# Kernel optimization log

Hardware: AMD Instinct MI355X
Metric: run time of the kernel (lower is better)

## Reference

```python
import jax, jax.numpy as jnp
import numpy as np

SEQLS = [256, 256, 256, 256]
HEADS = 8
DIM_HEAD = 64
DIM = 512
SCALE = DIM_HEAD ** -0.5
EPS = 1e-5
# static segment-id per token position: [N]
SEG = np.repeat(np.arange(len(SEQLS)), SEQLS)


def setup_inputs() -> dict:
    key = jax.random.key(0)
    k_x, k_m, k_qkv, k_out = jax.random.split(key, 4)
    B, N = 8, sum(SEQLS)
    inner = HEADS * DIM_HEAD
    x = jax.random.normal(k_x, (B, N, DIM), dtype=jnp.float32)
    m_labels = jax.random.randint(k_m, (B, len(SEQLS)), 0, 2)
    gamma = jnp.ones((DIM,), jnp.float32)
    beta = jnp.zeros((DIM,), jnp.float32)
    w_qkv = jax.random.normal(k_qkv, (DIM, 3 * inner), jnp.float32) * (DIM ** -0.5)
    w_out = jax.random.normal(k_out, (inner, DIM), jnp.float32) * (inner ** -0.5)
    b_out = jnp.zeros((DIM,), jnp.float32)
    return {"x": x, "m_labels": m_labels, "gamma": gamma, "beta": beta,
            "w_qkv": w_qkv, "w_out": w_out, "b_out": b_out}


def reference(x, m_labels, gamma, beta, w_qkv, w_out, b_out):
    B, N, _ = x.shape
    # LayerNorm
    mu = jnp.mean(x, axis=-1, keepdims=True)
    var = jnp.var(x, axis=-1, keepdims=True)
    h = (x - mu) * jax.lax.rsqrt(var + EPS) * gamma + beta
    # QKV projection (no bias)
    qkv = h @ w_qkv  # [B, N, 3*inner]
    q, k, v = jnp.split(qkv, 3, axis=-1)
    to_heads = lambda t: t.reshape(B, N, HEADS, DIM_HEAD).transpose(0, 2, 1, 3)
    q, k, v = to_heads(q), to_heads(k), to_heads(v)  # [B, H, N, D]
    dots = jnp.einsum('bhid,bhjd->bhij', q, k) * SCALE  # [B, H, N, N]
    # modality-block additive mask: -inf on any row/col of a missing modality
    missing = (m_labels == 0)[:, SEG]  # [B, N]
    blocked = missing[:, :, None] | missing[:, None, :]  # [B, N, N]
    dots = jnp.where(blocked[:, None, :, :], -jnp.inf, dots)
    # custom softmax: rows that are fully -inf output 0
    all_inf = jnp.all(jnp.isinf(dots), axis=-1, keepdims=True)
    safe = jnp.where(all_inf, 0.0, dots)
    attn = jax.nn.softmax(safe, axis=-1)
    attn = jnp.where(all_inf, 0.0, attn)
    out = jnp.einsum('bhij,bhjd->bhid', attn, v)  # [B, H, N, D]
    out = out.transpose(0, 2, 1, 3).reshape(B, N, HEADS * DIM_HEAD)
    return out @ w_out + b_out
```

## Files before the change

### kernel.cpp

```cpp
#include <hip/hip_runtime.h>

typedef _Float16 f16;
typedef _Float16 f16x8 __attribute__((ext_vector_type(8)));
typedef float f32x4 __attribute__((ext_vector_type(4)));

typedef __attribute__((address_space(1))) void gvoid;
typedef __attribute__((address_space(3))) void lvoid;
#define GLD16(gp, lp) __builtin_amdgcn_global_load_lds((gvoid*)(gp), (lvoid*)(lp), 16, 0, 0)

__device__ __forceinline__ f32x4 mfma16(f16x8 a, f16x8 b, f32x4 c) {
    return __builtin_amdgcn_mfma_f32_16x16x32_f16(a, b, c, 0, 0, 0);
}

__global__ __launch_bounds__(256) void k_prep(
    const float* __restrict__ x, const float* __restrict__ gamma,
    const float* __restrict__ beta, const int* __restrict__ mlab,
    const float* __restrict__ wqkv, const float* __restrict__ wout,
    f16* __restrict__ h, f16* __restrict__ wqkvT, f16* __restrict__ woutT)
{
    __shared__ float t[64][65];
    int bid = blockIdx.x, tid = threadIdx.x;
    if (bid < 2048) {
        int row = bid * 4 + (tid >> 6);
        int b = row >> 10, seg = (row >> 8) & 3;
        if (mlab[b * 4 + seg] == 0) return;
        int lane = tid & 63;
        const float* xr = x + (size_t)row * 512;
        float4 a = ((const float4*)xr)[lane * 2];
        float4 bv = ((const float4*)xr)[lane * 2 + 1];
        float v[8] = {a.x, a.y, a.z, a.w, bv.x, bv.y, bv.z, bv.w};
        float s = 0.f, s2 = 0.f;
#pragma unroll
        for (int j = 0; j < 8; ++j) { s += v[j]; s2 += v[j] * v[j]; }
#pragma unroll
        for (int off = 1; off < 64; off <<= 1) {
            s  += __shfl_xor(s, off);
            s2 += __shfl_xor(s2, off);
        }
        float mu  = s * (1.f / 512.f);
        float var = s2 * (1.f / 512.f) - mu * mu;
        float rstd = rsqrtf(var + 1e-5f);
        float4 g0 = ((const float4*)gamma)[lane * 2];
        float4 g1 = ((const float4*)gamma)[lane * 2 + 1];
        float4 b0 = ((const float4*)beta)[lane * 2];
        float4 b1 = ((const float4*)beta)[lane * 2 + 1];
        float g[8]  = {g0.x, g0.y, g0.z, g0.w, g1.x, g1.y, g1.z, g1.w};
        float bb[8] = {b0.x, b0.y, b0.z, b0.w, b1.x, b1.y, b1.z, b1.w};
        f16x8 o;
#pragma unroll
        for (int j = 0; j < 8; ++j) o[j] = (f16)((v[j] - mu) * rstd * g[j] + bb[j]);
        *(f16x8*)&h[(size_t)row * 512 + lane * 8] = o;
        return;
    }
    const float* in; f16* out; int C, c0, r0;
    if (bid < 2240) { int idx = bid - 2048; in = wqkv; out = wqkvT; C = 1536; c0 = (idx % 24) * 64; r0 = (idx / 24) * 64; }
    else            { int idx = bid - 2240; in = wout; out = woutT; C = 512;  c0 = (idx % 8)  * 64; r0 = (idx / 8)  * 64; }
#pragma unroll
    for (int i = 0; i < 16; ++i) {
        int r = i * 4 + (tid >> 6), c = tid & 63;
        t[r][c] = in[(size_t)(r0 + r) * C + c0 + c];
    }
    __syncthreads();
#pragma unroll
    for (int i = 0; i < 16; ++i) {
        int cr = i * 4 + (tid >> 6), cc = tid & 63;
        out[(size_t)(c0 + cr) * 512 + r0 + cc] = (f16)t[cc][cr];
    }
}

__global__ __launch_bounds__(256, 3) void k_gemm_qkv(
    const f16* __restrict__ A, const f16* __restrict__ Bt, const int* __restrict__ mlab,
    f16* __restrict__ q, f16* __restrict__ kmat, f16* __restrict__ vt)
{
    __shared__ __align__(16) f16 SM[24576];
    int tid = threadIdx.x, wid = tid >> 6, lane = tid & 63;
    int wm = wid >> 1, wn = wid & 1;
    int l15 = lane & 15, l4 = lane >> 4;
    int rowBase = blockIdx.y * 64;
    int colBase = blockIdx.x * 128;
    if (mlab[(rowBase >> 10) * 4 + ((rowBase & 1023) >> 8)] == 0) return;

    int srow = lane >> 3;
    int scolz = ((lane & 7) ^ srow) << 3;
    int kxor = (l15 & 7) << 3;

#define STG(bi, kt)                                                                              \
    do {                                                                                         \
        _Pragma("unroll") for (int i_ = 0; i_ < 2; ++i_) {                                       \
            int rg = (wid * 2 + i_) * 8;                                                         \
            GLD16(&A[(size_t)(rowBase + rg + srow) * 512 + (kt) + scolz], SM + (bi)*4096 + rg*64);\
        }                                                                                        \
        _Pragma("unroll") for (int i_ = 0; i_ < 4; ++i_) {                                       \
            int rg = (wid * 4 + i_) * 8;                                                         \
            GLD16(&Bt[(size_t)(colBase + rg + srow) * 512 + (kt) + scolz], SM + 8192 + (bi)*8192 + rg*64);\
        }                                                                                        \
    } while (0)

    f32x4 acc[2][4] = {};
    STG(0, 0);
    for (int ki = 0; ki < 8; ++ki) {
        int bi = ki & 1;
        __syncthreads();
        if (ki < 7) STG(bi ^ 1, (ki + 1) * 64);
#pragma unroll
        for (int kk = 0; kk < 2; ++kk) {
            f16x8 af[2], bf[4];
#pragma unroll
            for (int m = 0; m < 2; ++m)
                af[m] = *(const f16x8*)&SM[bi*4096 + (wm * 32 + m * 16 + l15) * 64 + ((kk * 32 + l4 * 8) ^ kxor)];
#pragma unroll
            for (int n = 0; n < 4; ++n)
                bf[n] = *(const f16x8*)&SM[8192 + bi*8192 + (wn * 64 + n * 16 + l15) * 64 + ((kk * 32 + l4 * 8) ^ kxor)];
#pragma unroll
            for (int m = 0; m < 2; ++m)
#pragma unroll
                for (int n = 0; n < 4; ++n)
                    acc[m][n] = mfma16(af[m], bf[n], acc[m][n]);
        }
    }
#undef STG

    __syncthreads();
    bool isV = (colBase >= 1024);
    if (!isV) {
#pragma unroll
        for (int m = 0; m < 2; ++m)
#pragma unroll
            for (int n = 0; n < 4; ++n)
#pragma unroll
                for (int r = 0; r < 4; ++r)
                    SM[(wm*32 + m*16 + l4*4 + r) * 136 + wn*64 + n*16 + l15] = (f16)acc[m][n][r];
        __syncthreads();
        int rl = tid >> 2, cl0 = (tid & 3) * 32;
        int row = rowBase + rl, bq = row >> 10, nt = row & 1023;
#pragma unroll
        for (int jj = 0; jj < 4; ++jj) {
            f16x8 v = *(const f16x8*)&SM[rl * 136 + cl0 + jj * 8];
            int col = colBase + cl0 + jj * 8;
            int which = col >> 9, hh2 = (col >> 6) & 7, d = col & 63;
            f16* dst = which ? kmat : q;
            *(f16x8*)&dst[((size_t)(bq * 8 + hh2) * 1024 + nt) * 64 + d] = v;
        }
    } else {
#pragma unroll
        for (int m = 0; m < 2; ++m)
#pragma unroll
            for (int n = 0; n < 4; ++n)
#pragma unroll
                for (int r = 0; r < 4; ++r)
                    SM[(wn*64 + n*16 + l15) * 72 + wm*32 + m*16 + l4*4 + r] = (f16)acc[m][n][r];
        __syncthreads();
        int cl = tid >> 1, rl0 = (tid & 1) * 32;
        int col = colBase + cl, hh2 = (col >> 6) & 7, d = col & 63;
        int bq = rowBase >> 10, ntb = (rowBase & 1023) + rl0;
        f16* dstrow = vt + ((size_t)(bq * 8 + hh2) * 64 + d) * 1024 + ntb;
#pragma unroll
        for (int jj = 0; jj < 4; ++jj)
            *(f16x8*)&dstrow[jj * 8] = *(const f16x8*)&SM[cl * 72 + rl0 + jj * 8];
    }
}

__global__ __launch_bounds__(512, 4) void k_attn(
    const f16* __restrict__ q, const f16* __restrict__ kmat,
    const f16* __restrict__ vt, const int* __restrict__ mlab,
    f16* __restrict__ ao)
{
    __shared__ __align__(16) f16 KV[32768];
    __shared__ float ML[512];

    int bid = blockIdx.x;
    int bh = (bid & 7) + 8 * (bid >> 7);
    int qb = (bid >> 3) & 15;
    int b = bh >> 3, hh = bh & 7;
    int tid = threadIdx.x, wid = tid >> 6, lane = tid & 63;
    int g = wid >> 1, qs = wid & 1;
    int l15 = lane & 15, l4 = lane >> 4;
    int qbase = qb * 64;
    size_t bhs = (size_t)bh;

    if (mlab[b * 4 + (qb >> 2)] == 0) return;

    unsigned ps = 0; int npres = 0;
#pragma unroll
    for (int s = 0; s < 4; ++s)
        if (mlab[b * 4 + s] != 0) { ps |= (unsigned)s << (4 * npres); ++npres; }
    int niter = npres * 2;
#define T0C(c) ((int)((ps >> (4 * ((c) >> 3))) & 15) * 256 + ((c) & 7) * 32)

    f16x8 qf0[2], qf1[2];
#pragma unroll
    for (int kk = 0; kk < 2; ++kk) {
        qf0[kk] = *(const f16x8*)&q[(bhs * 1024 + qbase + qs * 32 + l15) * 64 + kk * 32 + l4 * 8];
        qf1[kk] = *(const f16x8*)&q[(bhs * 1024 + qbase + qs * 32 + 16 + l15) * 64 + kk * 32 + l4 * 8];
#pragma unroll
        for (int j = 0; j < 8; ++j) { qf0[kk][j] = qf0[kk][j] * (f16)0.125; qf1[kk][j] = qf1[kk][j] * (f16)0.125; }
    }

    int sA = qs * 64 + lane, sB = sA + 128;
    int krA = sA >> 3, kcA = ((sA & 7) ^ (krA & 7)) << 3;
    int krB = sB >> 3, kcB = ((sB & 7) ^ (krB & 7)) << 3;
    int vrA = sA >> 2, vcA = ((sA & 3) ^ ((vrA >> 1) & 3)) << 3;
    int vrB = sB >> 2, vcB = ((sB & 3) ^ ((vrB >> 1) & 3)) << 3;
    const f16* kgA = kmat + (bhs * 1024 + krA) * 64 + kcA;
    const f16* kgB = kmat + (bhs * 1024 + krB) * 64 + kcB;
    const f16* vgA = vt + (bhs * 64 + vrA) * 1024 + vcA;
    const f16* vgB = vt + (bhs * 64 + vrB) * 1024 + vcB;

#define STAGE(bi, t0)                                                \
    do {                                                             \
        f16* kd = KV + (g * 2 + (bi)) * 2048 + qs * 512;             \
        f16* vd = KV + 16384 + (g * 2 + (bi)) * 2048 + qs * 512;     \
        GLD16(kgA + (size_t)(t0) * 64, kd);                          \
        GLD16(kgB + (size_t)(t0) * 64, kd + 1024);                   \
        GLD16(vgA + (t0), vd);                                       \
        GLD16(vgB + (t0), vd + 1024);                                \
    } while (0)

    float mrun0 = -1e30f, mrun1 = -1e30f, lrun0 = 0.f, lrun1 = 0.f;
    f32x4 o0[4] = {}, o1[4] = {};
    int kxor = l15 & 7;
    int vxor = (l15 >> 1) & 3;
    int srcA = l15 + ((l4 & 1) * 2) * 16, srcB = srcA + 16;
    int sel = l4 >> 1;

    STAGE(0, T0C(g));

    for (int i = 0; i < niter; ++i) {
        int bi = i & 1;
        __syncthreads();
        if (i + 1 < niter) STAGE(bi ^ 1, T0C(4 * (i + 1) + g));

        const f16* Kt = KV + (g * 2 + bi) * 2048;
        const f16* Vt = KV + 16384 + (g * 2 + bi) * 2048;

        f32x4 s00 = {}, s01 = {}, s10 = {}, s11 = {};
        __builtin_amdgcn_s_setprio(1);
#pragma unroll
        for (int kk = 0; kk < 2; ++kk) {
            f16x8 ka0 = *(const f16x8*)&Kt[(0 * 16 + l15) * 64 + (((kk * 4 + l4) ^ kxor) << 3)];
            f16x8 ka1 = *(const f16x8*)&Kt[(1 * 16 + l15) * 64 + (((kk * 4 + l4) ^ kxor) << 3)];
            s00 = mfma16(ka0, qf0[kk], s00);
            s10 = mfma16(ka0, qf1[kk], s10);
            s01 = mfma16(ka1, qf0[kk], s01);
            s11 = mfma16(ka1, qf1[kk], s11);
        }
        __builtin_amdgcn_s_setprio(0);

        union PK { f16 h[4]; long long ll; };
        union PB { long long ll[2]; f16x8 v; } pb0, pb1;
        {
            f32x4 mm;
#pragma unroll
            for (int r = 0; r < 4; ++r) mm[r] = fmaxf(s00[r], s01[r]);
            float mx = fmaxf(fmaxf(mm[0], mm[1]), fmaxf(mm[2], mm[3]));
            mx = fmaxf(mx, __shfl_xor(mx, 16));
            mx = fmaxf(mx, __shfl_xor(mx, 32));
            float mnew = fmaxf(mrun0, mx);
            float alpha = __expf(mrun0 - mnew);
            mrun0 = mnew;
            float rs = 0.f;
            PK pk0, pk1;
#pragma unroll
            for (int r = 0; r < 4; ++r) {
                float p0 = __expf(s00[r] - mnew), p1 = __expf(s01[r] - mnew);
                rs += p0 + p1;
                pk0.h[r] = (f16)p0; pk1.h[r] = (f16)p1;
            }
            rs += __shfl_xor(rs, 16);
            rs += __shfl_xor(rs, 32);
            lrun0 = lrun0 * alpha + rs;
#pragma unroll
            for (int nd = 0; nd < 4; ++nd) o0[nd] *= alpha;
            long long A0 = __shfl(pk0.ll, srcA), A1 = __shfl(pk1.ll, srcA);
            long long B0 = __shfl(pk0.ll, srcB), B1 = __shfl(pk1.ll, srcB);
            pb0.ll[0] = sel ? A1 : A0;
            pb0.ll[1] = sel ? B1 : B0;
        }
        {
            f32x4 mm;
#pragma unroll
            for (int r = 0; r < 4; ++r) mm[r] = fmaxf(s10[r], s11[r]);
            float mx = fmaxf(fmaxf(mm[0], mm[1]), fmaxf(mm[2], mm[3]));
            mx = fmaxf(mx, __shfl_xor(mx, 16));
            mx = fmaxf(mx, __shfl_xor(mx, 32));
            float mnew = fmaxf(mrun1, mx);
            float alpha = __expf(mrun1 - mnew);
            mrun1 = mnew;
            float rs = 0.f;
            PK pk0, pk1;
#pragma unroll
            for (int r = 0; r < 4; ++r) {
                float p0 = __expf(s10[r] - mnew), p1 = __expf(s11[r] - mnew);
                rs += p0 + p1;
                pk0.h[r] = (f16)p0; pk1.h[r] = (f16)p1;
            }
            rs += __shfl_xor(rs, 16);
            rs += __shfl_xor(rs, 32);
            lrun1 = lrun1 * alpha + rs;
#pragma unroll
            for (int nd = 0; nd < 4; ++nd) o1[nd] *= alpha;
            long long A0 = __shfl(pk0.ll, srcA), A1 = __shfl(pk1.ll, srcA);
            long long B0 = __shfl(pk0.ll, srcB), B1 = __shfl(pk1.ll, srcB);
            pb1.ll[0] = sel ? A1 : A0;
            pb1.ll[1] = sel ? B1 : B0;
        }
        __builtin_amdgcn_s_setprio(1);
#pragma unroll
        for (int nd = 0; nd < 4; ++nd) {
            f16x8 va = *(const f16x8*)&Vt[(nd * 16 + l15) * 32 + ((l4 ^ vxor) << 3)];
            o0[nd] = mfma16(va, pb0.v, o0[nd]);
            o1[nd] = mfma16(va, pb1.v, o1[nd]);
        }
        __builtin_amdgcn_s_setprio(0);
    }
#undef STAGE
#undef T0C

    __syncthreads();
    float* mg = (float*)KV;
    int q0 = qs * 32 + l15;
    if (l4 == 0) {
        ML[g * 64 + q0] = mrun0;       ML[256 + g * 64 + q0] = lrun0;
        ML[g * 64 + q0 + 16] = mrun1;  ML[256 + g * 64 + q0 + 16] = lrun1;
    }
    {
        int xr0 = (q0 & 7) << 2, q1 = q0 + 16, xr1 = (q1 & 7) << 2;
#pragma unroll
        for (int nd = 0; nd < 4; ++nd) {
            *(f32x4*)&mg[g * 4096 + q0 * 64 + ((nd * 16 + l4 * 4) ^ xr0)] = o0[nd];
            *(f32x4*)&mg[g * 4096 + q1 * 64 + ((nd * 16 + l4 * 4) ^ xr1)] = o1[nd];
        }
    }
    __syncthreads();

    {
        int qq = l15 + l4 * 16;
        float m0 = ML[qq], m1 = ML[64 + qq], m2 = ML[128 + qq], m3 = ML[192 + qq];
        float M = fmaxf(fmaxf(m0, m1), fmaxf(m2, m3));
        float e0 = __expf(m0 - M), e1 = __expf(m1 - M), e2 = __expf(m2 - M), e3 = __expf(m3 - M);
        float L = ML[256 + qq] * e0 + ML[320 + qq] * e1 + ML[384 + qq] * e2 + ML[448 + qq] * e3;
        float inv = 1.f / L;
        int xr = (qq & 7) << 2;
        int Aoff = (wid * 8) ^ xr;
        f32x4 accA = {}, accB = {};
#pragma unroll
        for (int gg = 0; gg < 4; ++gg) {
            float eg = gg == 0 ? e0 : gg == 1 ? e1 : gg == 2 ? e2 : e3;
            f32x4 pa = *(const f32x4*)&mg[gg * 4096 + qq * 64 + Aoff];
            f32x4 pc = *(const f32x4*)&mg[gg * 4096 + qq * 64 + (Aoff ^ 4)];
#pragma unroll
            for (int r = 0; r < 4; ++r) { accA[r] += eg * pa[r]; accB[r] += eg * pc[r]; }
        }
        union { f16 h[8]; f16x8 v; } w;
#pragma unroll
        for (int r = 0; r < 4; ++r) {
            w.h[r] = (f16)(accA[r] * inv);
            w.h[4 + r] = (f16)(accB[r] * inv);
        }
        *(f16x8*)&ao[(size_t)(b * 1024 + qbase + qq) * 512 + hh * 64 + wid * 8] = w.v;
    }
}

__global__ __launch_bounds__(256, 3) void k_gemm_out(
    const f16* __restrict__ A, const f16* __restrict__ Bt, const int* __restrict__ mlab,
    const float* __restrict__ bias, float* __restrict__ out)
{
    __shared__ f16 As[2][64 * 64];
    __shared__ f16 Bs[2][128 * 64];
    int tid = threadIdx.x, wid = tid >> 6, lane = tid & 63;
    int wm = wid >> 1, wn = wid & 1;
    int l15 = lane & 15, l4 = lane >> 4;
    int rowBase = blockIdx.y * 64;
    int colBase = blockIdx.x * 128;
    if (mlab[(rowBase >> 10) * 4 + ((rowBase & 1023) >> 8)] == 0) {
        for (int i = tid; i < 64 * 128; i += 256)
            out[(size_t)(rowBase + (i >> 7)) * 512 + colBase + (i & 127)] = bias[colBase + (i & 127)];
        return;
    }

    int srow = lane >> 3;
    int scolz = ((lane & 7) ^ srow) << 3;
    int kxor = (l15 & 7) << 3;

#define STG(bi, kt)                                                                         \
    do {                                                                                    \
        _Pragma("unroll") for (int i_ = 0; i_ < 2; ++i_) {                                  \
            int rg = (wid * 2 + i_) * 8;                                                    \
            GLD16(&A[(size_t)(rowBase + rg + srow) * 512 + (kt) + scolz], &As[bi][rg * 64]);\
        }                                                                                   \
        _Pragma("unroll") for (int i_ = 0; i_ < 4; ++i_) {                                  \
            int rg = (wid * 4 + i_) * 8;                                                    \
            GLD16(&Bt[(size_t)(colBase + rg + srow) * 512 + (kt) + scolz], &Bs[bi][rg * 64]);\
        }                                                                                   \
    } while (0)

    f32x4 acc[2][4] = {};
    STG(0, 0);
    for (int ki = 0; ki < 8; ++ki) {
        int bi = ki & 1;
        __syncthreads();
        if (ki < 7) STG(bi ^ 1, (ki + 1) * 64);
#pragma unroll
        for (int kk = 0; kk < 2; ++kk) {
            f16x8 af[2], bf[4];
#pragma unroll
            for (int m = 0; m < 2; ++m)
                af[m] = *(const f16x8*)&As[bi][(wm * 32 + m * 16 + l15) * 64 + ((kk * 32 + l4 * 8) ^ kxor)];
#pragma unroll
            for (int n = 0; n < 4; ++n)
                bf[n] = *(const f16x8*)&Bs[bi][(wn * 64 + n * 16 + l15) * 64 + ((kk * 32 + l4 * 8) ^ kxor)];
#pragma unroll
            for (int m = 0; m < 2; ++m)
#pragma unroll
                for (int n = 0; n < 4; ++n)
                    acc[m][n] = mfma16(af[m], bf[n], acc[m][n]);
        }
    }
#undef STG
#pragma unroll
    for (int m = 0; m < 2; ++m)
#pragma unroll
        for (int n = 0; n < 4; ++n)
#pragma unroll
            for (int r = 0; r < 4; ++r) {
                int row = rowBase + wm * 32 + m * 16 + l4 * 4 + r;
                int col = colBase + wn * 64 + n * 16 + l15;
                out[(size_t)row * 512 + col] = acc[m][n][r] + bias[col];
            }
}

extern "C" void kernel_launch(void* const* d_in, const int* in_sizes, int n_in,
                              void* d_out, int out_size, void* d_ws, size_t ws_size,
                              hipStream_t stream) {
    const float* x     = (const float*)d_in[0];
    const int*   mlab  = (const int*)d_in[1];
    const float* gamma = (const float*)d_in[2];
    const float* beta  = (const float*)d_in[3];
    const float* wqkv  = (const float*)d_in[4];
    const float* wout  = (const float*)d_in[5];
    const float* bout  = (const float*)d_in[6];
    float* out = (float*)d_out;

    f16* h     = (f16*)d_ws;
    f16* wqkvT = h + 8192 * 512;
    f16* woutT = wqkvT + 1536 * 512;
    f16* q     = woutT + 512 * 512;
    f16* kmat  = q + 4 * 1024 * 1024;
    f16* vt    = kmat + 4 * 1024 * 1024;
    f16* ao    = h;

    k_prep<<<2304, 256, 0, stream>>>(x, gamma, beta, mlab, wqkv, wout, h, wqkvT, woutT);
    k_gemm_qkv<<<dim3(12, 128), 256, 0, stream>>>(h, wqkvT, mlab, q, kmat, vt);
    k_attn<<<1024, 512, 0, stream>>>(q, kmat, vt, mlab, ao);
    k_gemm_out<<<dim3(4, 128), 256, 0, stream>>>(ao, woutT, mlab, bout, out);
}
```

Baseline: 62.15 us.

## Shrink attention KV tiles to 16 keys to raise occupancy

Each attention wave group now handles 16-key tiles instead of 32, and the PV product moves to the 16x16x16 MFMA so the P fragment can be used directly without cross-lane shuffles. LDS for the K/V tiles is halved and the cross-group merge buffer is stored as f16 rather than f32. The launch bound rises from 4 to 6 blocks per CU to use the freed LDS and registers. In exchange there are twice as many loop iterations and barriers per block, smaller MFMAs, and the partial outputs lose precision when stored as f16 before the merge.

```diff
diff --git a/kernel.cpp b/kernel.cpp
--- a/kernel.cpp
+++ b/kernel.cpp
@@ -1,6 +1,7 @@
 #include <hip/hip_runtime.h>
 
 typedef _Float16 f16;
+typedef _Float16 f16x4 __attribute__((ext_vector_type(4)));
 typedef _Float16 f16x8 __attribute__((ext_vector_type(8)));
 typedef float f32x4 __attribute__((ext_vector_type(4)));
 
@@ -10,6 +11,9 @@
 
 __device__ __forceinline__ f32x4 mfma16(f16x8 a, f16x8 b, f32x4 c) {
     return __builtin_amdgcn_mfma_f32_16x16x32_f16(a, b, c, 0, 0, 0);
+}
+__device__ __forceinline__ f32x4 mfma16k16(f16x4 a, f16x4 b, f32x4 c) {
+    return __builtin_amdgcn_mfma_f32_16x16x16f16(a, b, c, 0, 0, 0);
 }
 
 __global__ __launch_bounds__(256) void k_prep(
@@ -160,12 +164,12 @@
     }
 }
 
-__global__ __launch_bounds__(512, 4) void k_attn(
+__global__ __launch_bounds__(512, 6) void k_attn(
     const f16* __restrict__ q, const f16* __restrict__ kmat,
     const f16* __restrict__ vt, const int* __restrict__ mlab,
     f16* __restrict__ ao)
 {
-    __shared__ __align__(16) f16 KV[32768];
+    __shared__ __align__(16) f16 KV[16384];
     __shared__ float ML[512];
 
     int bid = blockIdx.x;
@@ -184,8 +188,8 @@
 #pragma unroll
     for (int s = 0; s < 4; ++s)
         if (mlab[b * 4 + s] != 0) { ps |= (unsigned)s << (4 * npres); ++npres; }
-    int niter = npres * 2;
-#define T0C(c) ((int)((ps >> (4 * ((c) >> 3))) & 15) * 256 + ((c) & 7) * 32)
+    int niter = npres * 4;
+#define T0C(c) ((int)((ps >> (4 * ((c) >> 4))) & 15) * 256 + ((c) & 15) * 16)
 
     f16x8 qf0[2], qf1[2];
 #pragma unroll
@@ -196,32 +200,21 @@
         for (int j = 0; j < 8; ++j) { qf0[kk][j] = qf0[kk][j] * (f16)0.125; qf1[kk][j] = qf1[kk][j] * (f16)0.125; }
     }
 
-    int sA = qs * 64 + lane, sB = sA + 128;
-    int krA = sA >> 3, kcA = ((sA & 7) ^ (krA & 7)) << 3;
-    int krB = sB >> 3, kcB = ((sB & 7) ^ (krB & 7)) << 3;
-    int vrA = sA >> 2, vcA = ((sA & 3) ^ ((vrA >> 1) & 3)) << 3;
-    int vrB = sB >> 2, vcB = ((sB & 3) ^ ((vrB >> 1) & 3)) << 3;
-    const f16* kgA = kmat + (bhs * 1024 + krA) * 64 + kcA;
-    const f16* kgB = kmat + (bhs * 1024 + krB) * 64 + kcB;
-    const f16* vgA = vt + (bhs * 64 + vrA) * 1024 + vcA;
-    const f16* vgB = vt + (bhs * 64 + vrB) * 1024 + vcB;
-
-#define STAGE(bi, t0)                                                \
-    do {                                                             \
-        f16* kd = KV + (g * 2 + (bi)) * 2048 + qs * 512;             \
-        f16* vd = KV + 16384 + (g * 2 + (bi)) * 2048 + qs * 512;     \
-        GLD16(kgA + (size_t)(t0) * 64, kd);                          \
-        GLD16(kgB + (size_t)(t0) * 64, kd + 1024);                   \
-        GLD16(vgA + (t0), vd);                                       \
-        GLD16(vgB + (t0), vd + 1024);                                \
+    int s0 = qs * 64 + lane;
+    int krow = s0 >> 3, kpos = (s0 & 7) ^ (krow & 7);
+    int vrow = s0 >> 1, vhalf = (s0 & 1) ^ ((s0 >> 3) & 1);
+    const f16* kg = kmat + (bhs * 1024 + krow) * 64 + kpos * 8;
+    const f16* vg = vt + (bhs * 64 + vrow) * 1024 + vhalf * 8;
+
+#define STAGE(bi, t0)                                            \
+    do {                                                         \
+        GLD16(kg + (size_t)(t0) * 64, KV + (g * 2 + (bi)) * 1024 + qs * 512);        \
+        GLD16(vg + (t0), KV + 8192 + (g * 2 + (bi)) * 1024 + qs * 512);              \
     } while (0)
 
     float mrun0 = -1e30f, mrun1 = -1e30f, lrun0 = 0.f, lrun1 = 0.f;
     f32x4 o0[4] = {}, o1[4] = {};
-    int kxor = l15 & 7;
-    int vxor = (l15 >> 1) & 3;
-    int srcA = l15 + ((l4 & 1) * 2) * 16, srcB = srcA + 16;
-    int sel = l4 >> 1;
+    int kx = l15 & 7;
 
     STAGE(0, T0C(g));
 
@@ -230,86 +223,69 @@
         __syncthreads();
         if (i + 1 < niter) STAGE(bi ^ 1, T0C(4 * (i + 1) + g));
 
-        const f16* Kt = KV + (g * 2 + bi) * 2048;
-        const f16* Vt = KV + 16384 + (g * 2 + bi) * 2048;
-
-        f32x4 s00 = {}, s01 = {}, s10 = {}, s11 = {};
+        const f16* Kt = KV + (g * 2 + bi) * 1024;
+        const f16* Vt = KV + 8192 + (g * 2 + bi) * 1024;
+
+        f32x4 s00 = {}, s10 = {};
         __builtin_amdgcn_s_setprio(1);
 #pragma unroll
         for (int kk = 0; kk < 2; ++kk) {
-            f16x8 ka0 = *(const f16x8*)&Kt[(0 * 16 + l15) * 64 + (((kk * 4 + l4) ^ kxor) << 3)];
-            f16x8 ka1 = *(const f16x8*)&Kt[(1 * 16 + l15) * 64 + (((kk * 4 + l4) ^ kxor) << 3)];
-            s00 = mfma16(ka0, qf0[kk], s00);
-            s10 = mfma16(ka0, qf1[kk], s10);
-            s01 = mfma16(ka1, qf0[kk], s01);
-            s11 = mfma16(ka1, qf1[kk], s11);
+            f16x8 ka = *(const f16x8*)&Kt[l15 * 64 + (((kk * 4 + l4) ^ kx) << 3)];
+            s00 = mfma16(ka, qf0[kk], s00);
+            s10 = mfma16(ka, qf1[kk], s10);
         }
         __builtin_amdgcn_s_setprio(0);
 
-        union PK { f16 h[4]; long long ll; };
-        union PB { long long ll[2]; f16x8 v; } pb0, pb1;
+        f16x4 pb0, pb1;
         {
-            f32x4 mm;
-#pragma unroll
-            for (int r = 0; r < 4; ++r) mm[r] = fmaxf(s00[r], s01[r]);
-            float mx = fmaxf(fmaxf(mm[0], mm[1]), fmaxf(mm[2], mm[3]));
+            float mx = fmaxf(fmaxf(s00[0], s00[1]), fmaxf(s00[2], s00[3]));
             mx = fmaxf(mx, __shfl_xor(mx, 16));
             mx = fmaxf(mx, __shfl_xor(mx, 32));
             float mnew = fmaxf(mrun0, mx);
             float alpha = __expf(mrun0 - mnew);
             mrun0 = mnew;
             float rs = 0.f;
-            PK pk0, pk1;
 #pragma unroll
             for (int r = 0; r < 4; ++r) {
-                float p0 = __expf(s00[r] - mnew), p1 = __expf(s01[r] - mnew);
-                rs += p0 + p1;
-                pk0.h[r] = (f16)p0; pk1.h[r] = (f16)p1;
+                float p = __expf(s00[r] - mnew);
+                rs += p;
+                pb0[r] = (f16)p;
             }
             rs += __shfl_xor(rs, 16);
             rs += __shfl_xor(rs, 32);
             lrun0 = lrun0 * alpha + rs;
 #pragma unroll
             for (int nd = 0; nd < 4; ++nd) o0[nd] *= alpha;
-            long long A0 = __shfl(pk0.ll, srcA), A1 = __shfl(pk1.ll, srcA);
-            long long B0 = __shfl(pk0.ll, srcB), B1 = __shfl(pk1.ll, srcB);
-            pb0.ll[0] = sel ? A1 : A0;
-            pb0.ll[1] = sel ? B1 : B0;
         }
         {
-            f32x4 mm;
-#pragma unroll
-            for (int r = 0; r < 4; ++r) mm[r] = fmaxf(s10[r], s11[r]);
-            float mx = fmaxf(fmaxf(mm[0], mm[1]), fmaxf(mm[2], mm[3]));
+            float mx = fmaxf(fmaxf(s10[0], s10[1]), fmaxf(s10[2], s10[3]));
             mx = fmaxf(mx, __shfl_xor(mx, 16));
             mx = fmaxf(mx, __shfl_xor(mx, 32));
             float mnew = fmaxf(mrun1, mx);
             float alpha = __expf(mrun1 - mnew);
             mrun1 = mnew;
             float rs = 0.f;
-            PK pk0, pk1;
 #pragma unroll
             for (int r = 0; r < 4; ++r) {
-                float p0 = __expf(s10[r] - mnew), p1 = __expf(s11[r] - mnew);
-                rs += p0 + p1;
-                pk0.h[r] = (f16)p0; pk1.h[r] = (f16)p1;
+                float p = __expf(s10[r] - mnew);
+                rs += p;
+                pb1[r] = (f16)p;
             }
             rs += __shfl_xor(rs, 16);
             rs += __shfl_xor(rs, 32);
             lrun1 = lrun1 * alpha + rs;
 #pragma unroll
             for (int nd = 0; nd < 4; ++nd) o1[nd] *= alpha;
-            long long A0 = __shfl(pk0.ll, srcA), A1 = __shfl(pk1.ll, srcA);
-            long long B0 = __shfl(pk0.ll, srcB), B1 = __shfl(pk1.ll, srcB);
-            pb1.ll[0] = sel ? A1 : A0;
-            pb1.ll[1] = sel ? B1 : B0;
-        }
+        }
+
         __builtin_amdgcn_s_setprio(1);
 #pragma unroll
         for (int nd = 0; nd < 4; ++nd) {
-            f16x8 va = *(const f16x8*)&Vt[(nd * 16 + l15) * 32 + ((l4 ^ vxor) << 3)];
-            o0[nd] = mfma16(va, pb0.v, o0[nd]);
-            o1[nd] = mfma16(va, pb1.v, o1[nd]);
+            int row = nd * 16 + l15;
+            int sub = (((l4 >> 1) ^ ((row >> 2) & 1)) << 1) | (l4 & 1);
+            f16x4 va = *(const f16x4*)&Vt[row * 16 + sub * 4];
+            o0[nd] = mfma16k16(va, pb0, o0[nd]);
+            o1[nd] = mfma16k16(va, pb1, o1[nd]);
         }
         __builtin_amdgcn_s_setprio(0);
     }
@@ -317,19 +293,19 @@
 #undef T0C
 
     __syncthreads();
-    float* mg = (float*)KV;
-    int q0 = qs * 32 + l15;
+    f16* mg = KV;
+    int q0 = qs * 32 + l15, q1 = q0 + 16;
     if (l4 == 0) {
         ML[g * 64 + q0] = mrun0;       ML[256 + g * 64 + q0] = lrun0;
-        ML[g * 64 + q0 + 16] = mrun1;  ML[256 + g * 64 + q0 + 16] = lrun1;
-    }
-    {
-        int xr0 = (q0 & 7) << 2, q1 = q0 + 16, xr1 = (q1 & 7) << 2;
-#pragma unroll
-        for (int nd = 0; nd < 4; ++nd) {
-            *(f32x4*)&mg[g * 4096 + q0 * 64 + ((nd * 16 + l4 * 4) ^ xr0)] = o0[nd];
-            *(f32x4*)&mg[g * 4096 + q1 * 64 + ((nd * 16 + l4 * 4) ^ xr1)] = o1[nd];
-        }
+        ML[g * 64 + q1] = mrun1;       ML[256 + g * 64 + q1] = lrun1;
+    }
+#pragma unroll
+    for (int nd = 0; nd < 4; ++nd) {
+        f16x4 w0, w1;
+#pragma unroll
+        for (int r = 0; r < 4; ++r) { w0[r] = (f16)o0[nd][r]; w1[r] = (f16)o1[nd][r]; }
+        *(f16x4*)&mg[g * 4096 + q0 * 64 + (((nd * 4 + l4) ^ (q0 & 7)) << 2)] = w0;
+        *(f16x4*)&mg[g * 4096 + q1 * 64 + (((nd * 4 + l4) ^ (q1 & 7)) << 2)] = w1;
     }
     __syncthreads();
 
@@ -340,16 +316,16 @@
         float e0 = __expf(m0 - M), e1 = __expf(m1 - M), e2 = __expf(m2 - M), e3 = __expf(m3 - M);
         float L = ML[256 + qq] * e0 + ML[320 + qq] * e1 + ML[384 + qq] * e2 + ML[448 + qq] * e3;
         float inv = 1.f / L;
-        int xr = (qq & 7) << 2;
-        int Aoff = (wid * 8) ^ xr;
+        int posA = ((wid * 2) ^ (qq & 7)) << 2;
+        int posB = ((wid * 2 + 1) ^ (qq & 7)) << 2;
         f32x4 accA = {}, accB = {};
 #pragma unroll
         for (int gg = 0; gg < 4; ++gg) {
             float eg = gg == 0 ? e0 : gg == 1 ? e1 : gg == 2 ? e2 : e3;
-            f32x4 pa = *(const f32x4*)&mg[gg * 4096 + qq * 64 + Aoff];
-            f32x4 pc = *(const f32x4*)&mg[gg * 4096 + qq * 64 + (Aoff ^ 4)];
-#pragma unroll
-            for (int r = 0; r < 4; ++r) { accA[r] += eg * pa[r]; accB[r] += eg * pc[r]; }
+            f16x4 pa = *(const f16x4*)&mg[gg * 4096 + qq * 64 + posA];
+            f16x4 pc = *(const f16x4*)&mg[gg * 4096 + qq * 64 + posB];
+#pragma unroll
+            for (int r = 0; r < 4; ++r) { accA[r] += eg * (float)pa[r]; accB[r] += eg * (float)pc[r]; }
         }
         union { f16 h[8]; f16x8 v; } w;
 #pragma unroll
```

Result: slower. 71.52 us (+15.1%).
